# Optimization experiments

Hardware: AMD Instinct MI355X
Metric: run time of the kernel (lower is better)

Reference implementation:

```python
import jax, jax.numpy as jnp
import numpy as np

B, IN, H = 16384, 1024, 1024


def setup_inputs() -> dict:
    key = jax.random.key(0)
    ks = jax.random.split(key, 16)
    stdv = 1.0 / np.sqrt(H)
    u = lambda k, shape: jax.random.uniform(k, shape, jnp.float32, -stdv, stdv)
    return {
        "input": jax.random.normal(ks[0], (B, IN), jnp.float32),
        "prev_h": jax.random.normal(ks[1], (B, H), jnp.float32),
        "prev_c": jax.random.normal(ks[2], (B, H), jnp.float32),
        "weight_xi": u(ks[3], (IN, H)), "weight_hi": u(ks[4], (H, H)),
        "weight_xf": u(ks[5], (IN, H)), "weight_hf": u(ks[6], (H, H)),
        "weight_xu": u(ks[7], (IN, H)), "weight_hu": u(ks[8], (H, H)),
        "weight_xo": u(ks[9], (IN, H)), "weight_ho": u(ks[10], (H, H)),
        "bias_i": u(ks[11], (H,)), "bias_f": u(ks[12], (H,)),
        "bias_o": u(ks[13], (H,)), "bias_u": u(ks[14], (H,)),
    }


def reference(input, prev_h, prev_c,
              weight_xi, weight_hi, weight_xf, weight_hf,
              weight_xu, weight_hu, weight_xo, weight_ho,
              bias_i, bias_f, bias_o, bias_u):
    i = jax.nn.sigmoid(input @ weight_xi + prev_h @ weight_hi + bias_i)
    f = jax.nn.sigmoid(input @ weight_xf + prev_h @ weight_hf + bias_f)
    o = jax.nn.sigmoid(input @ weight_xo + prev_h @ weight_ho + bias_o)
    u = jnp.tanh(input @ weight_xu + prev_h @ weight_hu + bias_u)
    c = f * prev_c + i * u
    h = o * jnp.tanh(c)
    return (h, c)
```

## Files before the change

### kernel.cpp

```cpp
#include <hip/hip_runtime.h>
#include <hip/hip_bf16.h>
#include <stdint.h>
#include <type_traits>


typedef short bf16x8 __attribute__((ext_vector_type(8)));
typedef unsigned short u16x8 __attribute__((ext_vector_type(8)));
typedef float f32x4 __attribute__((ext_vector_type(4)));

__device__ __forceinline__ unsigned short f2bf(float f) {
    union { float f; uint32_t u; } v; v.f = f;
    uint32_t r = v.u + 0x7FFFu + ((v.u >> 16) & 1u);
    return (unsigned short)(r >> 16);
}

__device__ __forceinline__ float fsig(float x) { return 1.0f / (1.0f + __expf(-x)); }
__device__ __forceinline__ float ftanh(float x) { return 2.0f * fsig(2.0f * x) - 1.0f; }

__global__ __launch_bounds__(256) void pack_a_kernel(const float* __restrict__ input,
                                                     const float* __restrict__ prev_h,
                                                     unsigned short* __restrict__ Apk) {
    long idx = (long)blockIdx.x * 256 + threadIdx.x;
    long e0 = idx * 8;
    int b = (int)(e0 >> 11);
    int k = (int)(e0 & 2047);
    const float* src = (k < 1024) ? (input + (size_t)b * 1024 + k)
                                  : (prev_h + (size_t)b * 1024 + (k - 1024));
    float4 lo = *(const float4*)src;
    float4 hi = *(const float4*)(src + 4);
    u16x8 o;
    o[0] = f2bf(lo.x); o[1] = f2bf(lo.y); o[2] = f2bf(lo.z); o[3] = f2bf(lo.w);
    o[4] = f2bf(hi.x); o[5] = f2bf(hi.y); o[6] = f2bf(hi.z); o[7] = f2bf(hi.w);
    *(u16x8*)(Apk + e0) = o;
}

__global__ __launch_bounds__(256) void pack_b_kernel(
        const float* __restrict__ wxi, const float* __restrict__ wxf,
        const float* __restrict__ wxo, const float* __restrict__ wxu,
        const float* __restrict__ whi, const float* __restrict__ whf,
        const float* __restrict__ who, const float* __restrict__ whu,
        unsigned short* __restrict__ Bpk) {
    int idx = blockIdx.x * 256 + threadIdx.x;
    int g  = idx >> 18;
    int r  = idx & 262143;
    int kc = r >> 10;
    int j  = r & 1023;
    const float* wx = (g == 0) ? wxi : (g == 1) ? wxf : (g == 2) ? wxo : wxu;
    const float* wh = (g == 0) ? whi : (g == 1) ? whf : (g == 2) ? who : whu;
    int k0 = kc * 8;
    const float* src = (k0 < 1024) ? (wx + (size_t)k0 * 1024 + j)
                                   : (wh + (size_t)(k0 - 1024) * 1024 + j);
    u16x8 o;
#pragma unroll
    for (int t = 0; t < 8; ++t) o[t] = f2bf(src[(size_t)t * 1024]);
    *(u16x8*)(Bpk + (((size_t)(g * 1024 + j)) << 11) + k0) = o;
}


#define GLL(gp, lp) __builtin_amdgcn_global_load_lds( \
        (__attribute__((address_space(1))) void*)(gp), \
        (__attribute__((address_space(3))) void*)(lp), 16, 0, 0)

#define BAR() do { asm volatile("" ::: "memory"); __builtin_amdgcn_s_barrier(); \
                   asm volatile("" ::: "memory"); } while (0)

__global__ __launch_bounds__(512, 2) void lstm_gemm_kernel(
        const unsigned short* __restrict__ Apk,
        const unsigned short* __restrict__ Bpk,
        const float* __restrict__ prev_c,
        const float* __restrict__ bi, const float* __restrict__ bf_,
        const float* __restrict__ bo, const float* __restrict__ bu,
        float* __restrict__ out_h, float* __restrict__ out_c) {
    __shared__ __align__(16) unsigned char smem[131072];
    const int tid = threadIdx.x;
    const int w = tid >> 6, l = tid & 63;
    const int lr = l & 15, s4 = l >> 4;
    const int wm = w >> 2, wq = w & 3;

    const int bid = blockIdx.x;
    const int sw = ((bid & 7) << 7) + (bid >> 3);
    const int tileRow = sw & 63, tileCol = sw >> 6;
    const int rowBase = tileRow * 256;
    const int jBase = tileCol * 64;

    const int swr = ((s4 ^ ((lr >> 1) & 3)) << 4);

    int aoff[8], boff[4];
#pragma unroll
    for (int m = 0; m < 8; ++m) aoff[m] = (wm * 128 + m * 16 + lr) * 64 + swr;
#pragma unroll
    for (int g = 0; g < 4; ++g) boff[g] = 16384 + (g * 64 + wq * 16 + lr) * 64 + swr;

    const int slot = (l & 3) ^ ((l >> 3) & 3);
    const int rloc = w * 16 + (l >> 2);
    const unsigned short* aSrc0 = Apk + (size_t)(rowBase + rloc) * 2048 + slot * 8;
    const unsigned short* aSrc1 = Apk + (size_t)(rowBase + 128 + rloc) * 2048 + slot * 8;
    const int br0 = rloc, br1 = 128 + rloc;
    const unsigned short* bSrc0 = Bpk + (((size_t)((br0 >> 6) * 1024 + jBase + (br0 & 63))) << 11) + slot * 8;
    const unsigned short* bSrc1 = Bpk + (((size_t)((br1 >> 6) * 1024 + jBase + (br1 & 63))) << 11) + slot * 8;
    const int aDst0 = w * 1024;
    const int aDst1 = 8192 + w * 1024;
    const int bDst0 = 16384 + w * 1024;
    const int bDst1 = 24576 + w * 1024;

#define STAGE4(T) do { const int _bb = ((T) & 3) * 32768; \
        GLL(aSrc0 + (size_t)(T) * 32, smem + _bb + aDst0); \
        GLL(aSrc1 + (size_t)(T) * 32, smem + _bb + aDst1); \
        GLL(bSrc0 + (size_t)(T) * 32, smem + _bb + bDst0); \
        GLL(bSrc1 + (size_t)(T) * 32, smem + _bb + bDst1); } while (0)

    f32x4 acc[8][4];
    const f32x4 vzero = {0.f, 0.f, 0.f, 0.f};
#pragma unroll
    for (int m = 0; m < 8; ++m)
#pragma unroll
        for (int g = 0; g < 4; ++g) acc[m][g] = vzero;

    STAGE4(0); STAGE4(1);
    asm volatile("s_waitcnt vmcnt(4)" ::: "memory");
    BAR();

    auto slice = [&](int t, auto vnc, auto stgc) {
        constexpr int VN = decltype(vnc)::value;
        constexpr bool STG = decltype(stgc)::value;
        const int bt = (t & 3) * 32768;
        if constexpr (STG) STAGE4(t + 2);
        bf16x8 bv[4], av[8];
#pragma unroll
        for (int g = 0; g < 4; ++g) bv[g] = *(const bf16x8*)(smem + bt + boff[g]);
#pragma unroll
        for (int m = 0; m < 8; ++m) av[m] = *(const bf16x8*)(smem + bt + aoff[m]);
#pragma unroll
        for (int m = 0; m < 8; ++m)
#pragma unroll
            for (int g = 0; g < 4; ++g)
                acc[m][g] = __builtin_amdgcn_mfma_f32_16x16x32_bf16(av[m], bv[g], acc[m][g], 0, 0, 0);
        if constexpr (VN == 4)      asm volatile("s_waitcnt vmcnt(4)" ::: "memory");
        else if constexpr (VN == 0) asm volatile("s_waitcnt vmcnt(0)" ::: "memory");
        if constexpr (VN >= 0) BAR();
    };

    using c4 = std::integral_constant<int, 4>;
    using c0 = std::integral_constant<int, 0>;
    using cm = std::integral_constant<int, -1>;
    using bT = std::integral_constant<bool, true>;
    using bF = std::integral_constant<bool, false>;

#pragma unroll 1
    for (int t = 0; t < 62; ++t) slice(t, c4{}, bT{});
    slice(62, c0{}, bF{});
    slice(63, cm{}, bF{});

    const int colIdx = jBase + wq * 16 + lr;
    const float vbi = bi[colIdx], vbf = bf_[colIdx], vbo = bo[colIdx], vbu = bu[colIdx];
    const int rowB = rowBase + wm * 128 + s4 * 4;
#pragma unroll
    for (int m = 0; m < 8; ++m) {
#pragma unroll
        for (int tt = 0; tt < 4; ++tt) {
            const size_t idx = (size_t)(rowB + m * 16 + tt) * 1024 + colIdx;
            float zi = acc[m][0][tt] + vbi;
            float zf = acc[m][1][tt] + vbf;
            float zo = acc[m][2][tt] + vbo;
            float zu = acc[m][3][tt] + vbu;
            float iv = fsig(zi), fv = fsig(zf), ov = fsig(zo), uv = ftanh(zu);
            float cv = fv * prev_c[idx] + iv * uv;
            out_c[idx] = cv;
            out_h[idx] = ov * ftanh(cv);
        }
    }
#undef STAGE4
}

extern "C" void kernel_launch(void* const* d_in, const int* in_sizes, int n_in,
                              void* d_out, int out_size, void* d_ws, size_t ws_size,
                              hipStream_t stream) {
    const float* input  = (const float*)d_in[0];
    const float* prev_h = (const float*)d_in[1];
    const float* prev_c = (const float*)d_in[2];
    const float* wxi = (const float*)d_in[3];
    const float* whi = (const float*)d_in[4];
    const float* wxf = (const float*)d_in[5];
    const float* whf = (const float*)d_in[6];
    const float* wxu = (const float*)d_in[7];
    const float* whu = (const float*)d_in[8];
    const float* wxo = (const float*)d_in[9];
    const float* who = (const float*)d_in[10];
    const float* bi  = (const float*)d_in[11];
    const float* bf_ = (const float*)d_in[12];
    const float* bo  = (const float*)d_in[13];
    const float* bu  = (const float*)d_in[14];

    unsigned short* Apk = (unsigned short*)d_ws;
    unsigned short* Bpk = (unsigned short*)((char*)d_ws + (size_t)67108864);

    float* out_h = (float*)d_out;
    float* out_c = out_h + (size_t)16384 * 1024;

    pack_a_kernel<<<dim3(16384), dim3(256), 0, stream>>>(input, prev_h, Apk);
    pack_b_kernel<<<dim3(4096), dim3(256), 0, stream>>>(wxi, wxf, wxo, wxu,
                                                        whi, whf, who, whu, Bpk);
    lstm_gemm_kernel<<<dim3(1024), dim3(512), 0, stream>>>(Apk, Bpk, prev_c,
                                                           bi, bf_, bo, bu, out_h, out_c);
}
```

Before: 345.1 us.

## Shrink GEMM block tile to 128 rows with 4 waves and 3-stage LDS ring

The fused LSTM GEMM block tile shrinks from 256x(4x64) to 128x(4x64). Each block now runs 4 waves instead of 8, and the grid doubles to 2048 blocks. The LDS ring drops from 4 buffers of 32KB to 3 buffers of 24KB, with staging issued 2 slices ahead and each thread issuing 6 async global-to-LDS loads per stage. The aim is to cut LDS use so more blocks fit per CU and to balance work across more blocks, at the cost of less B reuse per block and more global traffic.

Measured after the change: 378.8 us. 9.7% more time.

```diff
diff --git a/kernel.cpp b/kernel.cpp
--- a/kernel.cpp
+++ b/kernel.cpp
@@ -64,50 +64,50 @@
 #define BAR() do { asm volatile("" ::: "memory"); __builtin_amdgcn_s_barrier(); \
                    asm volatile("" ::: "memory"); } while (0)
 
-__global__ __launch_bounds__(512, 2) void lstm_gemm_kernel(
+__global__ __launch_bounds__(256, 2) void lstm_gemm_kernel(
         const unsigned short* __restrict__ Apk,
         const unsigned short* __restrict__ Bpk,
         const float* __restrict__ prev_c,
         const float* __restrict__ bi, const float* __restrict__ bf_,
         const float* __restrict__ bo, const float* __restrict__ bu,
         float* __restrict__ out_h, float* __restrict__ out_c) {
-    __shared__ __align__(16) unsigned char smem[131072];
+    __shared__ __align__(16) unsigned char smem[73728];
     const int tid = threadIdx.x;
     const int w = tid >> 6, l = tid & 63;
     const int lr = l & 15, s4 = l >> 4;
-    const int wm = w >> 2, wq = w & 3;
+    const int wq = w;
 
     const int bid = blockIdx.x;
-    const int sw = ((bid & 7) << 7) + (bid >> 3);
-    const int tileRow = sw & 63, tileCol = sw >> 6;
-    const int rowBase = tileRow * 256;
+    const int sw = ((bid & 7) << 8) + (bid >> 3);
+    const int tileRow = sw & 127, tileCol = sw >> 7;
+    const int rowBase = tileRow * 128;
     const int jBase = tileCol * 64;
 
     const int swr = ((s4 ^ ((lr >> 1) & 3)) << 4);
 
     int aoff[8], boff[4];
 #pragma unroll
-    for (int m = 0; m < 8; ++m) aoff[m] = (wm * 128 + m * 16 + lr) * 64 + swr;
-#pragma unroll
-    for (int g = 0; g < 4; ++g) boff[g] = 16384 + (g * 64 + wq * 16 + lr) * 64 + swr;
-
-    const int slot = (l & 3) ^ ((l >> 3) & 3);
-    const int rloc = w * 16 + (l >> 2);
-    const unsigned short* aSrc0 = Apk + (size_t)(rowBase + rloc) * 2048 + slot * 8;
-    const unsigned short* aSrc1 = Apk + (size_t)(rowBase + 128 + rloc) * 2048 + slot * 8;
-    const int br0 = rloc, br1 = 128 + rloc;
-    const unsigned short* bSrc0 = Bpk + (((size_t)((br0 >> 6) * 1024 + jBase + (br0 & 63))) << 11) + slot * 8;
-    const unsigned short* bSrc1 = Bpk + (((size_t)((br1 >> 6) * 1024 + jBase + (br1 & 63))) << 11) + slot * 8;
-    const int aDst0 = w * 1024;
-    const int aDst1 = 8192 + w * 1024;
-    const int bDst0 = 16384 + w * 1024;
-    const int bDst1 = 24576 + w * 1024;
-
-#define STAGE4(T) do { const int _bb = ((T) & 3) * 32768; \
-        GLL(aSrc0 + (size_t)(T) * 32, smem + _bb + aDst0); \
-        GLL(aSrc1 + (size_t)(T) * 32, smem + _bb + aDst1); \
-        GLL(bSrc0 + (size_t)(T) * 32, smem + _bb + bDst0); \
-        GLL(bSrc1 + (size_t)(T) * 32, smem + _bb + bDst1); } while (0)
+    for (int m = 0; m < 8; ++m) aoff[m] = (m * 16 + lr) * 64 + swr;
+#pragma unroll
+    for (int g = 0; g < 4; ++g) boff[g] = 8192 + (g * 64 + wq * 16 + lr) * 64 + swr;
+
+    const int rloc = tid >> 2;
+    const int sigS = ((tid & 3) ^ ((rloc >> 1) & 3)) * 8;
+    const unsigned short* aS0 = Apk + (size_t)(rowBase +  0 + rloc) * 2048 + sigS;
+    const unsigned short* aS1 = Apk + (size_t)(rowBase + 64 + rloc) * 2048 + sigS;
+    const unsigned short* bS0 = Bpk + (((size_t)(0 * 1024 + jBase + rloc)) << 11) + sigS;
+    const unsigned short* bS1 = Bpk + (((size_t)(1 * 1024 + jBase + rloc)) << 11) + sigS;
+    const unsigned short* bS2 = Bpk + (((size_t)(2 * 1024 + jBase + rloc)) << 11) + sigS;
+    const unsigned short* bS3 = Bpk + (((size_t)(3 * 1024 + jBase + rloc)) << 11) + sigS;
+    const int wB = w * 1024;
+
+#define STAGE6(T) do { const int _bb = ((T) % 3) * 24576; \
+        GLL(aS0 + (size_t)(T) * 32, smem + _bb +     0 + wB); \
+        GLL(aS1 + (size_t)(T) * 32, smem + _bb +  4096 + wB); \
+        GLL(bS0 + (size_t)(T) * 32, smem + _bb +  8192 + wB); \
+        GLL(bS1 + (size_t)(T) * 32, smem + _bb + 12288 + wB); \
+        GLL(bS2 + (size_t)(T) * 32, smem + _bb + 16384 + wB); \
+        GLL(bS3 + (size_t)(T) * 32, smem + _bb + 20480 + wB); } while (0)
 
     f32x4 acc[8][4];
     const f32x4 vzero = {0.f, 0.f, 0.f, 0.f};
@@ -116,15 +116,15 @@
 #pragma unroll
         for (int g = 0; g < 4; ++g) acc[m][g] = vzero;
 
-    STAGE4(0); STAGE4(1);
-    asm volatile("s_waitcnt vmcnt(4)" ::: "memory");
+    STAGE6(0); STAGE6(1);
+    asm volatile("s_waitcnt vmcnt(6)" ::: "memory");
     BAR();
 
     auto slice = [&](int t, auto vnc, auto stgc) {
         constexpr int VN = decltype(vnc)::value;
         constexpr bool STG = decltype(stgc)::value;
-        const int bt = (t & 3) * 32768;
-        if constexpr (STG) STAGE4(t + 2);
+        const int bt = (t % 3) * 24576;
+        if constexpr (STG) STAGE6(t + 2);
         bf16x8 bv[4], av[8];
 #pragma unroll
         for (int g = 0; g < 4; ++g) bv[g] = *(const bf16x8*)(smem + bt + boff[g]);
@@ -135,25 +135,25 @@
 #pragma unroll
             for (int g = 0; g < 4; ++g)
                 acc[m][g] = __builtin_amdgcn_mfma_f32_16x16x32_bf16(av[m], bv[g], acc[m][g], 0, 0, 0);
-        if constexpr (VN == 4)      asm volatile("s_waitcnt vmcnt(4)" ::: "memory");
+        if constexpr (VN == 6)      asm volatile("s_waitcnt vmcnt(6)" ::: "memory");
         else if constexpr (VN == 0) asm volatile("s_waitcnt vmcnt(0)" ::: "memory");
         if constexpr (VN >= 0) BAR();
     };
 
-    using c4 = std::integral_constant<int, 4>;
+    using c6 = std::integral_constant<int, 6>;
     using c0 = std::integral_constant<int, 0>;
     using cm = std::integral_constant<int, -1>;
     using bT = std::integral_constant<bool, true>;
     using bF = std::integral_constant<bool, false>;
 
 #pragma unroll 1
-    for (int t = 0; t < 62; ++t) slice(t, c4{}, bT{});
+    for (int t = 0; t < 62; ++t) slice(t, c6{}, bT{});
     slice(62, c0{}, bF{});
     slice(63, cm{}, bF{});
 
     const int colIdx = jBase + wq * 16 + lr;
     const float vbi = bi[colIdx], vbf = bf_[colIdx], vbo = bo[colIdx], vbu = bu[colIdx];
-    const int rowB = rowBase + wm * 128 + s4 * 4;
+    const int rowB = rowBase + s4 * 4;
 #pragma unroll
     for (int m = 0; m < 8; ++m) {
 #pragma unroll
@@ -169,7 +169,7 @@
             out_h[idx] = ov * ftanh(cv);
         }
     }
-#undef STAGE4
+#undef STAGE6
 }
 
 extern "C" void kernel_launch(void* const* d_in, const int* in_sizes, int n_in,
@@ -200,6 +200,6 @@
     pack_a_kernel<<<dim3(16384), dim3(256), 0, stream>>>(input, prev_h, Apk);
     pack_b_kernel<<<dim3(4096), dim3(256), 0, stream>>>(wxi, wxf, wxo, wxu,
                                                         whi, whf, who, whu, Bpk);
-    lstm_gemm_kernel<<<dim3(1024), dim3(512), 0, stream>>>(Apk, Bpk, prev_c,
+    lstm_gemm_kernel<<<dim3(2048), dim3(256), 0, stream>>>(Apk, Bpk, prev_c,
                                                            bi, bf_, bo, bu, out_h, out_c);
 }
```

## Switch to 32x32x16 MFMA with register double-buffered fragments and deeper prefetch

Applied to the files above, without the earlier changes.

Replaces the 16x16x32 bf16 MFMA tiling with 32x32x16 MFMAs and remaps the 8 waves to a 4x2 grid, so each wave owns 64 rows by 32 columns per gate. This cuts LDS fragment reads per unit of math. Fragments for the next K-slice are loaded into alternating register sets while the current slice's MFMAs run. The global-to-LDS prefetch depth grows from two slices ahead to three. The cost is more live registers (two fragment sets plus 16-wide accumulators) and a rewritten epilogue index mapping for the 32x32 output layout.

New measurement: 360.2 us. 1.04x slower.

```diff
diff --git a/kernel.cpp b/kernel.cpp
--- a/kernel.cpp
+++ b/kernel.cpp
@@ -6,7 +6,7 @@
 
 typedef short bf16x8 __attribute__((ext_vector_type(8)));
 typedef unsigned short u16x8 __attribute__((ext_vector_type(8)));
-typedef float f32x4 __attribute__((ext_vector_type(4)));
+typedef float f32x16 __attribute__((ext_vector_type(16)));
 
 __device__ __forceinline__ unsigned short f2bf(float f) {
     union { float f; uint32_t u; } v; v.f = f;
@@ -74,8 +74,8 @@
     __shared__ __align__(16) unsigned char smem[131072];
     const int tid = threadIdx.x;
     const int w = tid >> 6, l = tid & 63;
-    const int lr = l & 15, s4 = l >> 4;
-    const int wm = w >> 2, wq = w & 3;
+    const int l31 = l & 31, l5 = l >> 5;
+    const int wr = w >> 1, wc = w & 1;
 
     const int bid = blockIdx.x;
     const int sw = ((bid & 7) << 7) + (bid >> 3);
@@ -83,58 +83,78 @@
     const int rowBase = tileRow * 256;
     const int jBase = tileCol * 64;
 
-    const int swr = ((s4 ^ ((lr >> 1) & 3)) << 4);
-
-    int aoff[8], boff[4];
-#pragma unroll
-    for (int m = 0; m < 8; ++m) aoff[m] = (wm * 128 + m * 16 + lr) * 64 + swr;
-#pragma unroll
-    for (int g = 0; g < 4; ++g) boff[g] = 16384 + (g * 64 + wq * 16 + lr) * 64 + swr;
-
-    const int slot = (l & 3) ^ ((l >> 3) & 3);
-    const int rloc = w * 16 + (l >> 2);
-    const unsigned short* aSrc0 = Apk + (size_t)(rowBase + rloc) * 2048 + slot * 8;
-    const unsigned short* aSrc1 = Apk + (size_t)(rowBase + 128 + rloc) * 2048 + slot * 8;
-    const int br0 = rloc, br1 = 128 + rloc;
-    const unsigned short* bSrc0 = Bpk + (((size_t)((br0 >> 6) * 1024 + jBase + (br0 & 63))) << 11) + slot * 8;
-    const unsigned short* bSrc1 = Bpk + (((size_t)((br1 >> 6) * 1024 + jBase + (br1 & 63))) << 11) + slot * 8;
-    const int aDst0 = w * 1024;
-    const int aDst1 = 8192 + w * 1024;
-    const int bDst0 = 16384 + w * 1024;
-    const int bDst1 = 24576 + w * 1024;
+    const int key = (l31 >> 1) & 3;
+    int aoff[2][2], boff[4][2];
+#pragma unroll
+    for (int m = 0; m < 2; ++m)
+#pragma unroll
+        for (int ks = 0; ks < 2; ++ks)
+            aoff[m][ks] = (wr * 64 + m * 32 + l31) * 64 + ((ks * 2 + l5) ^ key) * 16;
+#pragma unroll
+    for (int g = 0; g < 4; ++g)
+#pragma unroll
+        for (int ks = 0; ks < 2; ++ks)
+            boff[g][ks] = 16384 + (g * 64 + wc * 32 + l31) * 64 + ((ks * 2 + l5) ^ key) * 16;
+
+    const int rloc = tid >> 2;
+    const int sigS = ((l & 3) ^ ((l >> 3) & 3)) * 8;
+    const unsigned short* aS0 = Apk + (size_t)(rowBase +   0 + rloc) * 2048 + sigS;
+    const unsigned short* aS1 = Apk + (size_t)(rowBase + 128 + rloc) * 2048 + sigS;
+    const unsigned short* bS0 = Bpk + (((size_t)(((rloc >> 6) + 0) * 1024 + jBase + (rloc & 63))) << 11) + sigS;
+    const unsigned short* bS1 = Bpk + (((size_t)(((rloc >> 6) + 2) * 1024 + jBase + (rloc & 63))) << 11) + sigS;
+    const int wB = w * 1024;
 
 #define STAGE4(T) do { const int _bb = ((T) & 3) * 32768; \
-        GLL(aSrc0 + (size_t)(T) * 32, smem + _bb + aDst0); \
-        GLL(aSrc1 + (size_t)(T) * 32, smem + _bb + aDst1); \
-        GLL(bSrc0 + (size_t)(T) * 32, smem + _bb + bDst0); \
-        GLL(bSrc1 + (size_t)(T) * 32, smem + _bb + bDst1); } while (0)
-
-    f32x4 acc[8][4];
-    const f32x4 vzero = {0.f, 0.f, 0.f, 0.f};
-#pragma unroll
-    for (int m = 0; m < 8; ++m)
-#pragma unroll
-        for (int g = 0; g < 4; ++g) acc[m][g] = vzero;
-
-    STAGE4(0); STAGE4(1);
+        GLL(aS0 + (size_t)(T) * 32, smem + _bb +     0 + wB); \
+        GLL(aS1 + (size_t)(T) * 32, smem + _bb +  8192 + wB); \
+        GLL(bS0 + (size_t)(T) * 32, smem + _bb + 16384 + wB); \
+        GLL(bS1 + (size_t)(T) * 32, smem + _bb + 24576 + wB); } while (0)
+
+    f32x16 acc[2][4];
+#pragma unroll
+    for (int m = 0; m < 2; ++m)
+#pragma unroll
+        for (int g = 0; g < 4; ++g)
+#pragma unroll
+            for (int q = 0; q < 16; ++q) acc[m][g][q] = 0.f;
+
+    bf16x8 aE[4], bE[8], aO[4], bO[8];
+
+    auto ldfr = [&](int t, bf16x8 (&da)[4], bf16x8 (&db)[8]) {
+        const int bt = (t & 3) * 32768;
+#pragma unroll
+        for (int m = 0; m < 2; ++m)
+#pragma unroll
+            for (int ks = 0; ks < 2; ++ks)
+                da[m * 2 + ks] = *(const bf16x8*)(smem + bt + aoff[m][ks]);
+#pragma unroll
+        for (int g = 0; g < 4; ++g)
+#pragma unroll
+            for (int ks = 0; ks < 2; ++ks)
+                db[g * 2 + ks] = *(const bf16x8*)(smem + bt + boff[g][ks]);
+    };
+
+    STAGE4(0); STAGE4(1); STAGE4(2);
     asm volatile("s_waitcnt vmcnt(4)" ::: "memory");
     BAR();
-
-    auto slice = [&](int t, auto vnc, auto stgc) {
+    ldfr(0, aE, bE);
+
+    auto slice = [&](int t, auto vnc, auto stgc, auto nxtc,
+                     bf16x8 (&ca)[4], bf16x8 (&cb)[8],
+                     bf16x8 (&na)[4], bf16x8 (&nb)[8]) {
         constexpr int VN = decltype(vnc)::value;
         constexpr bool STG = decltype(stgc)::value;
-        const int bt = (t & 3) * 32768;
-        if constexpr (STG) STAGE4(t + 2);
-        bf16x8 bv[4], av[8];
-#pragma unroll
-        for (int g = 0; g < 4; ++g) bv[g] = *(const bf16x8*)(smem + bt + boff[g]);
-#pragma unroll
-        for (int m = 0; m < 8; ++m) av[m] = *(const bf16x8*)(smem + bt + aoff[m]);
-#pragma unroll
-        for (int m = 0; m < 8; ++m)
-#pragma unroll
-            for (int g = 0; g < 4; ++g)
-                acc[m][g] = __builtin_amdgcn_mfma_f32_16x16x32_bf16(av[m], bv[g], acc[m][g], 0, 0, 0);
+        constexpr bool NXT = decltype(nxtc)::value;
+        if constexpr (STG) STAGE4(t + 3);
+        if constexpr (NXT) ldfr(t + 1, na, nb);
+#pragma unroll
+        for (int ks = 0; ks < 2; ++ks)
+#pragma unroll
+            for (int m = 0; m < 2; ++m)
+#pragma unroll
+                for (int g = 0; g < 4; ++g)
+                    acc[m][g] = __builtin_amdgcn_mfma_f32_32x32x16_bf16(
+                        ca[m * 2 + ks], cb[g * 2 + ks], acc[m][g], 0, 0, 0);
         if constexpr (VN == 4)      asm volatile("s_waitcnt vmcnt(4)" ::: "memory");
         else if constexpr (VN == 0) asm volatile("s_waitcnt vmcnt(0)" ::: "memory");
         if constexpr (VN >= 0) BAR();
@@ -147,22 +167,28 @@
     using bF = std::integral_constant<bool, false>;
 
 #pragma unroll 1
-    for (int t = 0; t < 62; ++t) slice(t, c4{}, bT{});
-    slice(62, c0{}, bF{});
-    slice(63, cm{}, bF{});
-
-    const int colIdx = jBase + wq * 16 + lr;
+    for (int t = 0; t < 60; t += 2) {
+        slice(t,     c4{}, bT{}, bT{}, aE, bE, aO, bO);
+        slice(t + 1, c4{}, bT{}, bT{}, aO, bO, aE, bE);
+    }
+    slice(60, c4{}, bT{}, bT{}, aE, bE, aO, bO);
+    slice(61, c0{}, bF{}, bT{}, aO, bO, aE, bE);
+    slice(62, cm{}, bF{}, bT{}, aE, bE, aO, bO);
+    slice(63, cm{}, bF{}, bF{}, aO, bO, aE, bE);
+
+    const int colIdx = jBase + wc * 32 + l31;
     const float vbi = bi[colIdx], vbf = bf_[colIdx], vbo = bo[colIdx], vbu = bu[colIdx];
-    const int rowB = rowBase + wm * 128 + s4 * 4;
-#pragma unroll
-    for (int m = 0; m < 8; ++m) {
-#pragma unroll
-        for (int tt = 0; tt < 4; ++tt) {
-            const size_t idx = (size_t)(rowB + m * 16 + tt) * 1024 + colIdx;
-            float zi = acc[m][0][tt] + vbi;
-            float zf = acc[m][1][tt] + vbf;
-            float zo = acc[m][2][tt] + vbo;
-            float zu = acc[m][3][tt] + vbu;
+    const int rowB = rowBase + wr * 64 + 4 * l5;
+#pragma unroll
+    for (int m = 0; m < 2; ++m) {
+#pragma unroll
+        for (int q = 0; q < 16; ++q) {
+            const int row = rowB + m * 32 + (q & 3) + 8 * (q >> 2);
+            const size_t idx = (size_t)row * 1024 + colIdx;
+            float zi = acc[m][0][q] + vbi;
+            float zf = acc[m][1][q] + vbf;
+            float zo = acc[m][2][q] + vbo;
+            float zu = acc[m][3][q] + vbu;
             float iv = fsig(zi), fv = fsig(zf), ov = fsig(zo), uv = ftanh(zu);
             float cv = fv * prev_c[idx] + iv * uv;
             out_c[idx] = cv;
```
